# Kernel tuning notes

Measured on AMD Instinct MI355X. Metric: run time of the kernel, lower is better.

The kernel has to match this reference:

```python
import jax, jax.numpy as jnp
import numpy as np

ANCHORS = np.array([[10,13],[16,30],[33,23],[30,61],[62,45],[59,119],[116,90],[156,198],[373,326]], np.float32)
ANCHOR_MASK = [[6, 7, 8], [3, 4, 5], [0, 1, 2]]
INPUT_SHAPE = np.array([416, 416], np.float32)  # (h, w)
NUM_CLASSES = 80
EPS = 1e-7


def _bce(pred, target):
    # clip_by_tensor + binary cross entropy, as in the torch module
    p = jnp.clip(pred, EPS, 1.0 - EPS)
    return -target * jnp.log(p) - (1.0 - target) * jnp.log(1.0 - p)


def _box_iou(b1, b2):
    # b1: (..., 1, 4), b2: (..., n, 4), center-format xywh (normalized)
    b1_xy, b1_wh = b1[..., :2], b1[..., 2:4]
    b2_xy, b2_wh = b2[..., :2], b2[..., 2:4]
    b1_min, b1_max = b1_xy - b1_wh / 2.0, b1_xy + b1_wh / 2.0
    b2_min, b2_max = b2_xy - b2_wh / 2.0, b2_xy + b2_wh / 2.0
    inter_wh = jnp.maximum(jnp.minimum(b1_max, b2_max) - jnp.maximum(b1_min, b2_min), 0.0)
    inter = inter_wh[..., 0] * inter_wh[..., 1]
    a1 = b1_wh[..., 0] * b1_wh[..., 1]
    a2 = b2_wh[..., 0] * b2_wh[..., 1]
    return inter / (a1 + a2 - inter)


def _decode(y_pred, anchors):
    # y_pred: (b, 3*(5+C), h, w) -> raw: (b, 3, h, w, 5+C)
    b, _, h, w = y_pred.shape
    raw = y_pred.reshape(b, 3, 5 + NUM_CLASSES, h, w).transpose(0, 1, 3, 4, 2)
    gy, gx = jnp.meshgrid(jnp.arange(h, dtype=y_pred.dtype), jnp.arange(w, dtype=y_pred.dtype), indexing='ij')
    grid_xy = jnp.stack([gx, gy], axis=-1)  # (h, w, 2)
    pred_xy = jax.nn.sigmoid(raw[..., 0:2])
    pred_wh = raw[..., 2:4]                 # raw tw, th (MSE'd against log target)
    pred_conf = jax.nn.sigmoid(raw[..., 4:5])
    pred_class = jax.nn.sigmoid(raw[..., 5:])
    # decoded, normalized boxes for IoU-based negative mining
    box_xy = (pred_xy + grid_xy) / jnp.array([w, h], y_pred.dtype)
    box_wh = jnp.exp(pred_wh) * anchors.reshape(3, 1, 1, 2) / jnp.asarray(INPUT_SHAPE[::-1].copy())
    pred_box = jnp.concatenate([box_xy, box_wh], axis=-1)  # (b,3,h,w,4)
    return grid_xy, pred_box, pred_xy, pred_wh, pred_conf, pred_class


def _layer_loss(y_pred, y_true, target, anchors):
    b, _, h, w = y_pred.shape
    grid_xy, pred_box, pred_xy, pred_wh, pred_conf, pred_class = _decode(y_pred, anchors)
    object_mask = y_true[..., 4:5]
    true_xy = y_true[..., 0:2] * jnp.array([h, w], y_pred.dtype) - grid_xy
    true_wh = jnp.log(y_true[..., 2:4] * jnp.asarray(INPUT_SHAPE[::-1].copy()) / anchors.reshape(3, 1, 1, 2))
    true_wh = jnp.where(object_mask > 0, true_wh, jnp.zeros_like(true_wh))
    loss_scale = 2.0 - y_true[..., 2:3] * y_true[..., 3:4]
    # negative mask: every grid/anchor prediction vs all true boxes of its image (vectorized over batch)
    iou = _box_iou(pred_box[:, :, :, :, None, :], target[:, None, None, None, :, :4])  # (b,3,h,w,n)
    best_iou = jnp.max(iou, axis=-1)
    neg = (best_iou < 0.5).astype(y_pred.dtype)[..., None]
    neg_mask = (1.0 - object_mask) * neg
    loss_xy = jnp.sum(object_mask * loss_scale * _bce(pred_xy, true_xy))
    loss_wh = jnp.sum(object_mask * loss_scale * 0.5 * (pred_wh - true_wh) ** 2)
    conf_bce = _bce(pred_conf, object_mask)
    loss_conf = jnp.sum(object_mask * conf_bce) + jnp.sum(neg_mask * conf_bce)
    loss_cls = jnp.sum(object_mask * _bce(pred_class, y_true[..., 5:]))
    return loss_xy + loss_wh + loss_conf + loss_cls


def setup_inputs() -> dict:
    key = jax.random.key(0)
    ks = jax.random.split(key, 7)
    grids = [13, 26, 52]
    b, n = 32, 20
    inp = {}
    for i, g in enumerate(grids):
        inp[f'y_pred{i}'] = jax.random.normal(ks[i], (b, 3 * (5 + NUM_CLASSES), g, g), jnp.float32)
        # y_true values in (0.05, 0.95): keeps log(true_wh) and 1/y_true grads bounded
        inp[f'y_true{i}'] = 0.05 + 0.9 * jax.random.uniform(ks[3 + i], (b, 3, g, g, 5 + NUM_CLASSES), jnp.float32)
    inp['target'] = 0.05 + 0.9 * jax.random.uniform(ks[6], (b, n, 5), jnp.float32)
    return inp


def reference(y_pred0, y_pred1, y_pred2, y_true0, y_true1, y_true2, target):
    total = jnp.zeros((), jnp.float32)
    for yp, yt, mask in ((y_pred0, y_true0, ANCHOR_MASK[0]),
                         (y_pred1, y_true1, ANCHOR_MASK[1]),
                         (y_pred2, y_true2, ANCHOR_MASK[2])):
        total = total + _layer_loss(yp, yt, target, jnp.asarray(ANCHORS[mask]))
    return total
```

## Files before the change

kernel.cpp:

```cpp
#include <hip/hip_runtime.h>
#include <math.h>

#define BLOCK 256
#define NB0 64
#define NB1 254
#define NB2 1014
#define NBLOCKS (NB0 + NB1 + NB2)

typedef float f4a __attribute__((ext_vector_type(4), aligned(4)));

__constant__ float c_anch[9][2] = {
    {116.f, 90.f}, {156.f, 198.f}, {373.f, 326.f},
    { 30.f, 61.f}, { 62.f,  45.f}, { 59.f, 119.f},
    { 10.f, 13.f}, { 16.f,  30.f}, { 33.f,  23.f}
};

__device__ __forceinline__ float softplusf(float x) {
    float ax = fabsf(x);
    return fmaxf(x, 0.f) + __logf(1.f + __expf(-ax));
}

__device__ __forceinline__ float sigmoidf(float x) {
    return __fdividef(1.f, 1.f + __expf(-x));
}

__global__ __launch_bounds__(BLOCK) void yolo_loss_main(
    const float* __restrict__ p0, const float* __restrict__ p1, const float* __restrict__ p2,
    const float* __restrict__ t0, const float* __restrict__ t1, const float* __restrict__ t2,
    const float* __restrict__ tgt, float* __restrict__ partials)
{
    int blk = blockIdx.x;
    const float* pred;
    const float* tru;
    int layer, g, cells, bbase;
    if (blk < NB0)            { layer = 0; pred = p0; tru = t0; g = 13; cells = 16224;  bbase = 0; }
    else if (blk < NB0 + NB1) { layer = 1; pred = p1; tru = t1; g = 26; cells = 64896;  bbase = NB0; }
    else                      { layer = 2; pred = p2; tru = t2; g = 52; cells = 259584; bbase = NB0 + NB1; }

    int idx = (blk - bbase) * BLOCK + threadIdx.x;
    float acc = 0.f;

    if (idx < cells) {
        int hw = g * g;
        int ij = idx % hw;
        int a  = (idx / hw) % 3;
        int b  = idx / (3 * hw);
        int i  = ij / g;
        int j  = ij - i * g;

        const float* pb = pred + (size_t)((b * 3 + a) * 85) * hw + ij;
        const float* tb = tru + (size_t)((b * 3 + a) * hw + ij) * 85;

        float r0 = pb[0];
        float r1 = pb[hw];
        float r2 = pb[2 * hw];
        float r3 = pb[3 * hw];
        float r4 = pb[4 * hw];

        f4a y03 = *reinterpret_cast<const f4a*>(tb);
        float y0 = y03.x, y1 = y03.y, y2 = y03.z, y3 = y03.w;
        float mask = tb[4];

        float gf = (float)g, gx = (float)j, gy = (float)i;
        float aw = c_anch[layer * 3 + a][0];
        float ah = c_anch[layer * 3 + a][1];

        float true_x = y0 * gf - gx;
        float true_y = y1 * gf - gy;
        float ls = 2.f - y2 * y3;
        float lxy = (softplusf(r0) - true_x * r0) + (softplusf(r1) - true_y * r1);
        acc += mask * ls * lxy;

        float tw = __logf(y2 * (416.f / aw));
        float th = __logf(y3 * (416.f / ah));
        float dw = r2 - tw, dh = r3 - th;
        acc += mask * ls * 0.5f * (dw * dw + dh * dh);

        float cbce = softplusf(r4) - mask * r4;

        float sx = sigmoidf(r0);
        float sy = sigmoidf(r1);
        float bx = __fdividef(sx + gx, gf);
        float by = __fdividef(sy + gy, gf);
        float bw = __expf(r2) * aw * (1.f / 416.f);
        float bh = __expf(r3) * ah * (1.f / 416.f);
        float a1 = bw * bh;
        float b1minx = bx - 0.5f * bw, b1maxx = bx + 0.5f * bw;
        float b1miny = by - 0.5f * bh, b1maxy = by + 0.5f * bh;

        const float* tg = tgt + b * 20 * 5;
        float best = 0.f;
#pragma unroll 5
        for (int k = 0; k < 20; k++) {
            f4a t = *reinterpret_cast<const f4a*>(tg + k * 5);
            float hw2 = 0.5f * t.z, hh2 = 0.5f * t.w;
            float iw = fminf(b1maxx, t.x + hw2) - fmaxf(b1minx, t.x - hw2);
            float ih = fminf(b1maxy, t.y + hh2) - fmaxf(b1miny, t.y - hh2);
            iw = fmaxf(iw, 0.f);
            ih = fmaxf(ih, 0.f);
            float inter = iw * ih;
            float iou = __fdividef(inter, a1 + t.z * t.w - inter);
            best = fmaxf(best, iou);
        }
        float neg = (best < 0.5f) ? 1.f : 0.f;
        acc += mask * cbce + (1.f - mask) * neg * cbce;

        float cls = 0.f;
#pragma unroll 10
        for (int c4 = 0; c4 < 20; c4++) {
            f4a t = *reinterpret_cast<const f4a*>(tb + 5 + 4 * c4);
            const float* pc = pb + (size_t)(5 + 4 * c4) * hw;
            float x0 = pc[0];
            float x1 = pc[hw];
            float x2 = pc[2 * hw];
            float x3 = pc[3 * hw];
            cls += (softplusf(x0) - t.x * x0)
                 + (softplusf(x1) - t.y * x1)
                 + (softplusf(x2) - t.z * x2)
                 + (softplusf(x3) - t.w * x3);
        }
        acc += mask * cls;
    }

    for (int off = 32; off > 0; off >>= 1)
        acc += __shfl_down(acc, off, 64);
    __shared__ float sh[BLOCK / 64];
    if ((threadIdx.x & 63) == 0)
        sh[threadIdx.x >> 6] = acc;
    __syncthreads();
    if (threadIdx.x == 0) {
        float s = 0.f;
        for (int wv = 0; wv < BLOCK / 64; wv++) s += sh[wv];
        partials[blockIdx.x] = s;
    }
}

__global__ __launch_bounds__(BLOCK) void yolo_loss_reduce(
    const float* __restrict__ partials, float* __restrict__ out)
{
    float s = 0.f;
    for (int i = threadIdx.x; i < NBLOCKS; i += BLOCK)
        s += partials[i];
    for (int off = 32; off > 0; off >>= 1)
        s += __shfl_down(s, off, 64);
    __shared__ float sh[BLOCK / 64];
    if ((threadIdx.x & 63) == 0)
        sh[threadIdx.x >> 6] = s;
    __syncthreads();
    if (threadIdx.x == 0) {
        float tot = 0.f;
        for (int wv = 0; wv < BLOCK / 64; wv++) tot += sh[wv];
        out[0] = tot;
    }
}

extern "C" void kernel_launch(void* const* d_in, const int* in_sizes, int n_in,
                              void* d_out, int out_size, void* d_ws, size_t ws_size,
                              hipStream_t stream) {
    const float* p0  = (const float*)d_in[0];
    const float* t0  = (const float*)d_in[1];
    const float* p1  = (const float*)d_in[2];
    const float* t1  = (const float*)d_in[3];
    const float* p2  = (const float*)d_in[4];
    const float* t2  = (const float*)d_in[5];
    const float* tgt = (const float*)d_in[6];
    float* partials  = (float*)d_ws;

    yolo_loss_main<<<NBLOCKS, BLOCK, 0, stream>>>(p0, p1, p2, t0, t1, t2, tgt, partials);
    yolo_loss_reduce<<<1, BLOCK, 0, stream>>>(partials, (float*)d_out);
}
```

Baseline: 283.1 us.

## Stage y_true rows through shared memory for coalesced loads

The per-cell y_true reads, where each thread read an 85-float row at an 85-float stride, are replaced by cooperative block loads into a padded shared tile of 256x17. The first five fields and then five chunks of 16 class channels are staged, with barriers around each chunk. This turns strided per-thread loads into mostly contiguous block-wide loads, reducing wasted cache-line traffic on the largest input. It adds six barrier phases and about 17 KB of LDS per block, and the launch bounds now request 8 blocks per SIMD/CU, which may constrain registers.

```diff
diff --git a/kernel.cpp b/kernel.cpp
--- a/kernel.cpp
+++ b/kernel.cpp
@@ -24,11 +24,13 @@
     return __fdividef(1.f, 1.f + __expf(-x));
 }
 
-__global__ __launch_bounds__(BLOCK) void yolo_loss_main(
+__global__ __launch_bounds__(BLOCK, 8) void yolo_loss_main(
     const float* __restrict__ p0, const float* __restrict__ p1, const float* __restrict__ p2,
     const float* __restrict__ t0, const float* __restrict__ t1, const float* __restrict__ t2,
     const float* __restrict__ tgt, float* __restrict__ partials)
 {
+    __shared__ float sh[BLOCK][17];
+
     int blk = blockIdx.x;
     const float* pred;
     const float* tru;
@@ -37,29 +39,44 @@
     else if (blk < NB0 + NB1) { layer = 1; pred = p1; tru = t1; g = 26; cells = 64896;  bbase = NB0; }
     else                      { layer = 2; pred = p2; tru = t2; g = 52; cells = 259584; bbase = NB0 + NB1; }
 
-    int idx = (blk - bbase) * BLOCK + threadIdx.x;
+    int tid = threadIdx.x;
+    int cell0 = (blk - bbase) * BLOCK;
+    int idx = cell0 + tid;
+    bool active = idx < cells;
+    int nvalid = min(BLOCK, cells - cell0);
+    const float* trow = tru + (size_t)cell0 * 85;
+
+#pragma unroll
+    for (int k = 0; k < 5; k++) {
+        int f = k * BLOCK + tid;
+        int cell = f / 5;
+        int ch = f - cell * 5;
+        int cc = min(cell, nvalid - 1);
+        sh[cell][ch] = trow[(size_t)cc * 85 + ch];
+    }
+    __syncthreads();
+
+    int cidx = active ? idx : (cells - 1);
+    int hw = g * g;
+    int ij = cidx % hw;
+    int a  = (cidx / hw) % 3;
+    int b  = cidx / (3 * hw);
+    int i  = ij / g;
+    int j  = ij - i * g;
+    const float* pb = pred + (size_t)((b * 3 + a) * 85) * hw + ij;
+
     float acc = 0.f;
+    float mask = 0.f;
 
-    if (idx < cells) {
-        int hw = g * g;
-        int ij = idx % hw;
-        int a  = (idx / hw) % 3;
-        int b  = idx / (3 * hw);
-        int i  = ij / g;
-        int j  = ij - i * g;
-
-        const float* pb = pred + (size_t)((b * 3 + a) * 85) * hw + ij;
-        const float* tb = tru + (size_t)((b * 3 + a) * hw + ij) * 85;
+    if (active) {
+        float y0 = sh[tid][0], y1 = sh[tid][1], y2 = sh[tid][2], y3 = sh[tid][3];
+        mask = sh[tid][4];
 
         float r0 = pb[0];
         float r1 = pb[hw];
         float r2 = pb[2 * hw];
         float r3 = pb[3 * hw];
         float r4 = pb[4 * hw];
-
-        f4a y03 = *reinterpret_cast<const f4a*>(tb);
-        float y0 = y03.x, y1 = y03.y, y2 = y03.z, y3 = y03.w;
-        float mask = tb[4];
 
         float gf = (float)g, gx = (float)j, gy = (float)i;
         float aw = c_anch[layer * 3 + a][0];
@@ -104,33 +121,40 @@
         }
         float neg = (best < 0.5f) ? 1.f : 0.f;
         acc += mask * cbce + (1.f - mask) * neg * cbce;
+    }
 
-        float cls = 0.f;
-#pragma unroll 10
-        for (int c4 = 0; c4 < 20; c4++) {
-            f4a t = *reinterpret_cast<const f4a*>(tb + 5 + 4 * c4);
-            const float* pc = pb + (size_t)(5 + 4 * c4) * hw;
-            float x0 = pc[0];
-            float x1 = pc[hw];
-            float x2 = pc[2 * hw];
-            float x3 = pc[3 * hw];
-            cls += (softplusf(x0) - t.x * x0)
-                 + (softplusf(x1) - t.y * x1)
-                 + (softplusf(x2) - t.z * x2)
-                 + (softplusf(x3) - t.w * x3);
+    float cls = 0.f;
+    for (int q = 0; q < 5; q++) {
+        __syncthreads();
+#pragma unroll
+        for (int k = 0; k < 16; k++) {
+            int f = k * BLOCK + tid;
+            int cell = f >> 4;
+            int ch = f & 15;
+            int cc = min(cell, nvalid - 1);
+            sh[cell][ch] = trow[(size_t)cc * 85 + 5 + q * 16 + ch];
         }
-        acc += mask * cls;
+        __syncthreads();
+        if (active) {
+#pragma unroll
+            for (int c = 0; c < 16; c++) {
+                float x = pb[(size_t)(5 + q * 16 + c) * hw];
+                float t = sh[tid][c];
+                cls += softplusf(x) - t * x;
+            }
+        }
     }
+    if (active) acc += mask * cls;
 
     for (int off = 32; off > 0; off >>= 1)
         acc += __shfl_down(acc, off, 64);
-    __shared__ float sh[BLOCK / 64];
+    __shared__ float shr[BLOCK / 64];
     if ((threadIdx.x & 63) == 0)
-        sh[threadIdx.x >> 6] = acc;
+        shr[threadIdx.x >> 6] = acc;
     __syncthreads();
     if (threadIdx.x == 0) {
         float s = 0.f;
-        for (int wv = 0; wv < BLOCK / 64; wv++) s += sh[wv];
+        for (int wv = 0; wv < BLOCK / 64; wv++) s += shr[wv];
         partials[blockIdx.x] = s;
     }
 }
```

Result: no change. 288.1 us (+1.8%).

## Stage y_true through LDS per wave for coalesced loads, one wave per block

Applied to the files above, without the earlier changes.

Each block is now a single 64-lane wave handling 256 cells (4 per lane). The wave loads the cell-major y_true rows cooperatively in coalesced fashion into LDS (header and 8-channel class chunks, with register prefetch of the next chunk) and then reads them transposed. Before, each thread read a strided 85-float row. This targets poor coalescing of y_true reads, but it adds LDS traffic, higher register pressure (52 prefetch registers) and far fewer threads per block, which may hurt occupancy and latency hiding.

```diff
diff --git a/kernel.cpp b/kernel.cpp
--- a/kernel.cpp
+++ b/kernel.cpp
@@ -1,7 +1,6 @@
 #include <hip/hip_runtime.h>
 #include <math.h>
 
-#define BLOCK 256
 #define NB0 64
 #define NB1 254
 #define NB2 1014
@@ -24,59 +23,98 @@
     return __fdividef(1.f, 1.f + __expf(-x));
 }
 
-__global__ __launch_bounds__(BLOCK) void yolo_loss_main(
-    const float* __restrict__ p0, const float* __restrict__ p1, const float* __restrict__ p2,
-    const float* __restrict__ t0, const float* __restrict__ t1, const float* __restrict__ t2,
-    const float* __restrict__ tgt, float* __restrict__ partials)
+template<int G, int LAYER>
+__device__ __forceinline__ float wave_task(
+    const float* __restrict__ pred, const float* __restrict__ tru,
+    const float* __restrict__ tgt, int task, int cells, int lane,
+    float* __restrict__ S5, float* __restrict__ S9)
 {
-    int blk = blockIdx.x;
-    const float* pred;
-    const float* tru;
-    int layer, g, cells, bbase;
-    if (blk < NB0)            { layer = 0; pred = p0; tru = t0; g = 13; cells = 16224;  bbase = 0; }
-    else if (blk < NB0 + NB1) { layer = 1; pred = p1; tru = t1; g = 26; cells = 64896;  bbase = NB0; }
-    else                      { layer = 2; pred = p2; tru = t2; g = 52; cells = 259584; bbase = NB0 + NB1; }
-
-    int idx = (blk - bbase) * BLOCK + threadIdx.x;
+    constexpr int HW = G * G;
+    constexpr int CPB = 3 * HW;
+    const int cell0 = task * 256;
+    const int nv = cells - cell0;
+    const int nvc = min(nv, 256);
+    const float* tw = tru + (size_t)cell0 * 85;
+
+    float gate[4], gxv[4], gyv[4], awv[4], ahv[4];
+    int pbo[4], bb[4];
+#pragma unroll
+    for (int r = 0; r < 4; r++) {
+        int li = lane + 64 * r;
+        gate[r] = (li < nv) ? 1.f : 0.f;
+        int c = cell0 + li;
+        if (c > cells - 1) c = cells - 1;
+        int b = c / CPB;
+        int rem = c - b * CPB;
+        int a = rem / HW;
+        int ij = rem - a * HW;
+        int i = ij / G;
+        int j = ij - i * G;
+        bb[r]  = b;
+        pbo[r] = ((b * 3 + a) * 85) * HW + ij;
+        gxv[r] = (float)j;
+        gyv[r] = (float)i;
+        awv[r] = c_anch[LAYER * 3 + a][0];
+        ahv[r] = c_anch[LAYER * 3 + a][1];
+    }
+
+    float hreg[20];
+#pragma unroll
+    for (int k = 0; k < 20; k++) {
+        int f = k * 64 + lane;
+        int cell = f / 5;
+        int ch = f - cell * 5;
+        int cc = min(cell, nvc - 1);
+        hreg[k] = tw[cc * 85 + ch];
+    }
+    float creg[32];
+#pragma unroll
+    for (int k = 0; k < 32; k++) {
+        int f = k * 64 + lane;
+        int cell = f >> 3;
+        int cc = min(cell, nvc - 1);
+        creg[k] = tw[cc * 85 + 5 + (f & 7)];
+    }
+#pragma unroll
+    for (int k = 0; k < 20; k++)
+        S5[k * 64 + lane] = hreg[k];
+
     float acc = 0.f;
-
-    if (idx < cells) {
-        int hw = g * g;
-        int ij = idx % hw;
-        int a  = (idx / hw) % 3;
-        int b  = idx / (3 * hw);
-        int i  = ij / g;
-        int j  = ij - i * g;
-
-        const float* pb = pred + (size_t)((b * 3 + a) * 85) * hw + ij;
-        const float* tb = tru + (size_t)((b * 3 + a) * hw + ij) * 85;
-
+    float maskg[4];
+
+#pragma unroll
+    for (int r = 0; r < 4; r++) {
+        int row = lane + 64 * r;
+        float y0 = S5[row * 5 + 0];
+        float y1 = S5[row * 5 + 1];
+        float y2 = S5[row * 5 + 2];
+        float y3 = S5[row * 5 + 3];
+        float mk = S5[row * 5 + 4];
+        maskg[r] = gate[r] * mk;
+
+        const float* pb = pred + (size_t)pbo[r];
         float r0 = pb[0];
-        float r1 = pb[hw];
-        float r2 = pb[2 * hw];
-        float r3 = pb[3 * hw];
-        float r4 = pb[4 * hw];
-
-        f4a y03 = *reinterpret_cast<const f4a*>(tb);
-        float y0 = y03.x, y1 = y03.y, y2 = y03.z, y3 = y03.w;
-        float mask = tb[4];
-
-        float gf = (float)g, gx = (float)j, gy = (float)i;
-        float aw = c_anch[layer * 3 + a][0];
-        float ah = c_anch[layer * 3 + a][1];
-
+        float r1 = pb[HW];
+        float r2 = pb[2 * HW];
+        float r3 = pb[3 * HW];
+        float r4 = pb[4 * HW];
+
+        float gf = (float)G, gx = gxv[r], gy = gyv[r];
+        float aw = awv[r], ah = ahv[r];
+
+        float tmp = 0.f;
         float true_x = y0 * gf - gx;
         float true_y = y1 * gf - gy;
         float ls = 2.f - y2 * y3;
         float lxy = (softplusf(r0) - true_x * r0) + (softplusf(r1) - true_y * r1);
-        acc += mask * ls * lxy;
-
-        float tw = __logf(y2 * (416.f / aw));
-        float th = __logf(y3 * (416.f / ah));
-        float dw = r2 - tw, dh = r3 - th;
-        acc += mask * ls * 0.5f * (dw * dw + dh * dh);
-
-        float cbce = softplusf(r4) - mask * r4;
+        tmp += mk * ls * lxy;
+
+        float twl = __logf(y2 * (416.f / aw));
+        float thl = __logf(y3 * (416.f / ah));
+        float dw = r2 - twl, dh = r3 - thl;
+        tmp += mk * ls * 0.5f * (dw * dw + dh * dh);
+
+        float cbce = softplusf(r4) - mk * r4;
 
         float sx = sigmoidf(r0);
         float sy = sigmoidf(r1);
@@ -88,7 +126,7 @@
         float b1minx = bx - 0.5f * bw, b1maxx = bx + 0.5f * bw;
         float b1miny = by - 0.5f * bh, b1maxy = by + 0.5f * bh;
 
-        const float* tg = tgt + b * 20 * 5;
+        const float* tg = tgt + bb[r] * 100;
         float best = 0.f;
 #pragma unroll 5
         for (int k = 0; k < 20; k++) {
@@ -103,53 +141,88 @@
             best = fmaxf(best, iou);
         }
         float neg = (best < 0.5f) ? 1.f : 0.f;
-        acc += mask * cbce + (1.f - mask) * neg * cbce;
-
-        float cls = 0.f;
-#pragma unroll 10
-        for (int c4 = 0; c4 < 20; c4++) {
-            f4a t = *reinterpret_cast<const f4a*>(tb + 5 + 4 * c4);
-            const float* pc = pb + (size_t)(5 + 4 * c4) * hw;
-            float x0 = pc[0];
-            float x1 = pc[hw];
-            float x2 = pc[2 * hw];
-            float x3 = pc[3 * hw];
-            cls += (softplusf(x0) - t.x * x0)
-                 + (softplusf(x1) - t.y * x1)
-                 + (softplusf(x2) - t.z * x2)
-                 + (softplusf(x3) - t.w * x3);
-        }
-        acc += mask * cls;
-    }
+        tmp += mk * cbce + (1.f - mk) * neg * cbce;
+
+        acc += gate[r] * tmp;
+    }
+
+    float cls[4] = {0.f, 0.f, 0.f, 0.f};
+    for (int q = 0; q < 10; q++) {
+#pragma unroll
+        for (int k = 0; k < 32; k++) {
+            int f = k * 64 + lane;
+            S9[(f >> 3) * 9 + (f & 7)] = creg[k];
+        }
+        if (q < 9) {
+#pragma unroll
+            for (int k = 0; k < 32; k++) {
+                int f = k * 64 + lane;
+                int cell = f >> 3;
+                int cc = min(cell, nvc - 1);
+                creg[k] = tw[cc * 85 + 5 + 8 * (q + 1) + (f & 7)];
+            }
+        }
+        int chbase = 5 + 8 * q;
+#pragma unroll
+        for (int r = 0; r < 4; r++) {
+            int row = lane + 64 * r;
+            const float* pb = pred + (size_t)pbo[r] + (size_t)chbase * HW;
+            float c8 = 0.f;
+#pragma unroll
+            for (int c = 0; c < 8; c++) {
+                float x = pb[(size_t)c * HW];
+                float t = S9[row * 9 + c];
+                c8 += softplusf(x) - t * x;
+            }
+            cls[r] += c8;
+        }
+    }
+#pragma unroll
+    for (int r = 0; r < 4; r++)
+        acc += maskg[r] * cls[r];
+
+    return acc;
+}
+
+__global__ __launch_bounds__(64, 2) void yolo_loss_main(
+    const float* __restrict__ p0, const float* __restrict__ p1, const float* __restrict__ p2,
+    const float* __restrict__ t0, const float* __restrict__ t1, const float* __restrict__ t2,
+    const float* __restrict__ tgt, float* __restrict__ partials)
+{
+    __shared__ float S5[256 * 5];
+    __shared__ float S9[256 * 9];
+
+    int blk = blockIdx.x;
+    int lane = threadIdx.x;
+    float acc;
+    if (blk < NB0)
+        acc = wave_task<13, 0>(p0, t0, tgt, blk, 16224, lane, S5, S9);
+    else if (blk < NB0 + NB1)
+        acc = wave_task<26, 1>(p1, t1, tgt, blk - NB0, 64896, lane, S5, S9);
+    else
+        acc = wave_task<52, 2>(p2, t2, tgt, blk - NB0 - NB1, 259584, lane, S5, S9);
 
     for (int off = 32; off > 0; off >>= 1)
         acc += __shfl_down(acc, off, 64);
-    __shared__ float sh[BLOCK / 64];
-    if ((threadIdx.x & 63) == 0)
-        sh[threadIdx.x >> 6] = acc;
-    __syncthreads();
-    if (threadIdx.x == 0) {
-        float s = 0.f;
-        for (int wv = 0; wv < BLOCK / 64; wv++) s += sh[wv];
-        partials[blockIdx.x] = s;
-    }
-}
-
-__global__ __launch_bounds__(BLOCK) void yolo_loss_reduce(
+    if (lane == 0)
+        partials[blk] = acc;
+}
+
+__global__ __launch_bounds__(256) void yolo_loss_reduce(
     const float* __restrict__ partials, float* __restrict__ out)
 {
     float s = 0.f;
-    for (int i = threadIdx.x; i < NBLOCKS; i += BLOCK)
+    for (int i = threadIdx.x; i < NBLOCKS; i += 256)
         s += partials[i];
     for (int off = 32; off > 0; off >>= 1)
         s += __shfl_down(s, off, 64);
-    __shared__ float sh[BLOCK / 64];
+    __shared__ float sh[256 / 64];
     if ((threadIdx.x & 63) == 0)
         sh[threadIdx.x >> 6] = s;
     __syncthreads();
     if (threadIdx.x == 0) {
         float tot = 0.f;
-        for (int wv = 0; wv < BLOCK / 64; wv++) tot += sh[wv];
+        for (int wv = 0; wv < 256 / 64; wv++) tot += sh[wv];
         out[0] = tot;
     }
 }
@@ -166,6 +239,6 @@
     const float* tgt = (const float*)d_in[6];
     float* partials  = (float*)d_ws;
 
-    yolo_loss_main<<<NBLOCKS, BLOCK, 0, stream>>>(p0, p1, p2, t0, t1, t2, tgt, partials);
-    yolo_loss_reduce<<<1, BLOCK, 0, stream>>>(partials, (float*)d_out);
-}
+    yolo_loss_main<<<NBLOCKS, 64, 0, stream>>>(p0, p1, p2, t0, t1, t2, tgt, partials);
+    yolo_loss_reduce<<<1, 256, 0, stream>>>(partials, (float*)d_out);
+}
```

Result: slower. 294.8 us (+4.1%).
